# Performance work log

Measured on AMD Instinct MI355X. Metric: run time of the kernel, lower is better.

Reference implementation:

```python
import jax, jax.numpy as jnp
import numpy as np

N_QUBITS = 12
DEPTH = 4
OUT_DIM = 4096
BATCH = 2048
M_IN = 4096


def setup_inputs() -> dict:
    key = jax.random.key(0)
    k1, k2 = jax.random.split(key)
    x = jax.random.normal(k1, (BATCH, M_IN), dtype=jnp.float32)
    w = jax.random.uniform(k2, (DEPTH, N_QUBITS, 3), dtype=jnp.float32) * (2.0 * np.pi)
    return {"x": x, "w": w}


def _rot_matrix(phi, theta, omega):
    # PennyLane Rot(phi, theta, omega) = RZ(omega) @ RY(theta) @ RZ(phi)
    c = jnp.cos(theta / 2)
    s = jnp.sin(theta / 2)
    m = jnp.stack([
        jnp.stack([jnp.exp(-1j * (phi + omega) / 2) * c, -jnp.exp(1j * (phi - omega) / 2) * s]),
        jnp.stack([jnp.exp(-1j * (phi - omega) / 2) * s, jnp.exp(1j * (phi + omega) / 2) * c]),
    ])
    return m.astype(jnp.complex64)


def _apply_1q(s, U, q):
    # s: (B,) + (2,)*n ; wire q lives on axis q+1 (wire 0 = MSB, default.qubit order)
    s = jnp.moveaxis(s, q + 1, -1)
    s = jnp.einsum('...j,ij->...i', s, U)
    return jnp.moveaxis(s, -1, q + 1)


def _cnot(s, c, t):
    # control wire c < target wire t; flip target axis on the control=1 slice
    p0 = s[(slice(None),) * (c + 1) + (0,)]
    p1 = jnp.flip(s[(slice(None),) * (c + 1) + (1,)], axis=t)  # axis t after removing axis c+1
    return jnp.stack([p0, p1], axis=c + 1)


def _layer(s, wl):
    n = N_QUBITS
    for i in range(n):
        s = _apply_1q(s, _rot_matrix(wl[i, 0], wl[i, 1], wl[i, 2]), i)
    for i in range(n):
        for j in range(i + 1, n):
            s = _cnot(s, i, j)
    return s


def reference(x, w):
    B, m = x.shape
    n = N_QUBITS
    # amplitude embedding: per-sample L2 normalize with uniform fallback
    norm = jnp.linalg.norm(x, axis=1, keepdims=True)
    ok = norm > 1e-10
    amp = jnp.where(ok, x / jnp.where(ok, norm, 1.0), 1.0 / np.sqrt(m))
    s = amp.astype(jnp.complex64).reshape((B,) + (2,) * n)
    for layer in range(DEPTH):
        s = _layer(s, w[layer])
    sv = s.reshape(B, -1)
    probs = sv.real ** 2 + sv.imag ** 2
    pn = probs[:, :OUT_DIM]
    tot = jnp.sum(pn, axis=1, keepdims=True)
    okp = tot > 1e-10
    out = jnp.where(okp, pn / jnp.where(okp, tot, 1.0), 1.0 / OUT_DIM)
    return out.astype(x.dtype)
```

## Files before the change

kernel.cpp:

```cpp
#include <hip/hip_runtime.h>
#include <math.h>

#define NQ 12
#define DIM 4096
#define NLAYER 4
#define NT 512

typedef float v2 __attribute__((ext_vector_type(2)));

__device__ __forceinline__ v2 mkv2(float a, float b) { v2 r; r.x = a; r.y = b; return r; }
__device__ __forceinline__ v2 sp(float a) { v2 r; r.x = a; r.y = a; return r; }
__device__ __forceinline__ v2 pkfma(v2 a, float b, v2 c) {
  return __builtin_elementwise_fma(a, sp(b), c);
}

__device__ __forceinline__ int sfun(int z) {
  z ^= z >> 1; z ^= z >> 2; z ^= z >> 4; z ^= z >> 8; return z & (DIM - 1);
}
__device__ __forceinline__ int swz(int s) {
  int m = s ^ ((s >> 6) & 63);
  return m ^ ((m >> 3) & 7);
}

__device__ __forceinline__ v2 block_reduce_sum2(v2 v, v2* red) {
  const int tid = threadIdx.x;
#pragma unroll
  for (int off = 32; off > 0; off >>= 1) {
    v.x += __shfl_down(v.x, off, 64);
    v.y += __shfl_down(v.y, off, 64);
  }
  if ((tid & 63) == 0) red[tid >> 6] = v;
  __syncthreads();
  if (tid == 0) {
    v2 s = sp(0.f);
#pragma unroll
    for (int i = 0; i < NT / 64; ++i) s += red[i];
    red[0] = s;
  }
  __syncthreads();
  v2 r = red[0];
  __syncthreads();
  return r;
}

__device__ __forceinline__ void apply_pair(v2& r0, v2& i0, v2& r1, v2& i1,
    const float2 u00, const float2 u01, const float2 u10, const float2 u11) {
  v2 nr0 = pkfma(i1, -u01.y, pkfma(r1, u01.x, pkfma(i0, -u00.y, r0 * sp(u00.x))));
  v2 ni0 = pkfma(r1,  u01.y, pkfma(i1, u01.x, pkfma(r0,  u00.y, i0 * sp(u00.x))));
  v2 nr1 = pkfma(i1, -u11.y, pkfma(r1, u11.x, pkfma(i0, -u10.y, r0 * sp(u10.x))));
  v2 ni1 = pkfma(r1,  u11.y, pkfma(i1, u11.x, pkfma(r0,  u10.y, i0 * sp(u10.x))));
  r0 = nr0; i0 = ni0; r1 = nr1; i1 = ni1;
}

template <int RT>
__device__ __forceinline__ void gates3(v2 re[8], v2 im[8], const float2* GL) {
#pragma unroll
  for (int i = 0; i < 3; ++i) {
    const int q = 2 + 3 * RT - i;
    const float2 u00 = GL[q * 4 + 0], u01 = GL[q * 4 + 1];
    const float2 u10 = GL[q * 4 + 2], u11 = GL[q * 4 + 3];
#pragma unroll
    for (int pe = 0; pe < 4; ++pe) {
      const int e0 = ((pe >> i) << (i + 1)) | (pe & ((1 << i) - 1));
      const int e1 = e0 | (1 << i);
      apply_pair(re[e0], im[e0], re[e1], im[e1], u00, u01, u10, u11);
    }
  }
}

__global__ __launch_bounds__(NT, 4) void qsim_kernel(
    const float* __restrict__ x, const float* __restrict__ w,
    float* __restrict__ out) {
  extern __shared__ __align__(16) char smem[];
  float4* st   = (float4*)smem;
  float2* gmat = (float2*)(st + DIM);
  v2*     red  = (v2*)(gmat + NLAYER * NQ * 4);

  const int t = threadIdx.x;
  const int lane = t & 63, wave = t >> 6;
  const int a = t & 7, b = (t >> 3) & 7;
  const long r0 = 2L * blockIdx.x;

  if (t < NLAYER * NQ) {
    const float* wp = w + t * 3;
    float phi = wp[0], th = wp[1], om = wp[2];
    float sn, cc, sa, ca, sb, cb;
    sincosf(0.5f * th, &sn, &cc);
    sincosf(0.5f * (phi + om), &sa, &ca);
    sincosf(0.5f * (phi - om), &sb, &cb);
    float2* g = &gmat[t * 4];
    g[0] = make_float2(ca * cc, -sa * cc);
    g[1] = make_float2(-cb * sn, -sb * sn);
    g[2] = make_float2(cb * sn, -sb * sn);
    g[3] = make_float2(ca * cc, sa * cc);
  }

  const float4* xa = (const float4*)(x + r0 * DIM) + t * 2;
  const float4* xb = (const float4*)(x + (r0 + 1) * DIM) + t * 2;
  const float4 a0 = xa[0], a1 = xa[1], b0 = xb[0], b1 = xb[1];
  const float va[8] = {a0.x, a0.y, a0.z, a0.w, a1.x, a1.y, a1.z, a1.w};
  const float vb[8] = {b0.x, b0.y, b0.z, b0.w, b1.x, b1.y, b1.z, b1.w};
  v2 ss = sp(0.f);
#pragma unroll
  for (int e = 0; e < 8; ++e) { ss.x += va[e] * va[e]; ss.y += vb[e] * vb[e]; }
  const v2 nsq = block_reduce_sum2(ss, red);
  const float n0 = sqrtf(nsq.x), n1 = sqrtf(nsq.y);
  const bool ok0 = n0 > 1e-10f, ok1 = n1 > 1e-10f;
  const float i0f = ok0 ? 1.0f / n0 : 0.f, i1f = ok1 ? 1.0f / n1 : 0.f;
#pragma unroll
  for (int e = 0; e < 8; ++e)
    st[swz(t * 8 + e)] = make_float4(ok0 ? va[e] * i0f : 0.015625f,
                                     ok1 ? vb[e] * i1f : 0.015625f, 0.f, 0.f);

  int radr[8], gadr[8];
#pragma unroll
  for (int j = 0; j < 8; ++j) {
    radr[j] = swz(t | (j << 9));
    gadr[j] = swz(sfun(t | (j << 9)));
  }
  __syncthreads();

  v2 re[8], im[8];
#pragma unroll
  for (int L = 0; L < NLAYER; ++L) {
    const float2* GL = &gmat[L * NQ * 4];

#pragma unroll
    for (int j = 0; j < 8; ++j) {
      const float4 v = st[L == 0 ? radr[j] : gadr[j]];
      re[j] = mkv2(v.x, v.y); im[j] = mkv2(v.z, v.w);
    }
    gates3<0>(re, im, GL);
    __syncthreads();
#pragma unroll
    for (int j = 0; j < 8; ++j)
      st[swz(lane | (j << 6) | (wave << 9))] =
          make_float4(re[j].x, re[j].y, im[j].x, im[j].y);
    __syncthreads();

#pragma unroll
    for (int j = 0; j < 8; ++j) {
      const float4 v = st[radr[j]];
      re[j] = mkv2(v.x, v.y); im[j] = mkv2(v.z, v.w);
    }
    gates3<1>(re, im, GL);
    __syncthreads();
#pragma unroll
    for (int j = 0; j < 8; ++j)
      st[swz(a | (j << 3) | (wave << 6) | (b << 9))] =
          make_float4(re[j].x, re[j].y, im[j].x, im[j].y);
    __syncthreads();

#pragma unroll
    for (int j = 0; j < 8; ++j) {
      const float4 v = st[radr[j]];
      re[j] = mkv2(v.x, v.y); im[j] = mkv2(v.z, v.w);
    }
    gates3<2>(re, im, GL);
    __syncthreads();
#pragma unroll
    for (int j = 0; j < 8; ++j)
      st[swz(b | (j << 3) | (wave << 6) | (a << 9))] =
          make_float4(re[j].x, re[j].y, im[j].x, im[j].y);
    __syncthreads();

#pragma unroll
    for (int j = 0; j < 8; ++j) {
      const float4 v = st[radr[j]];
      re[j] = mkv2(v.x, v.y); im[j] = mkv2(v.z, v.w);
    }
    gates3<3>(re, im, GL);
    __syncthreads();
#pragma unroll
    for (int j = 0; j < 8; ++j)
      st[swz(j | (b << 3) | (a << 6) | (wave << 9))] =
          make_float4(re[j].x, re[j].y, im[j].x, im[j].y);
    __syncthreads();
  }

  float p0[8], p1[8];
  v2 ps = sp(0.f);
#pragma unroll
  for (int k = 0; k < 8; ++k) {
    const float4 v = st[gadr[k]];
    p0[k] = v.x * v.x + v.z * v.z;
    p1[k] = v.y * v.y + v.w * v.w;
    ps.x += p0[k]; ps.y += p1[k];
  }
  const v2 tot = block_reduce_sum2(ps, red);
  const bool k0 = tot.x > 1e-10f, k1 = tot.y > 1e-10f;
  const float t0 = k0 ? 1.0f / tot.x : 0.f, t1 = k1 ? 1.0f / tot.y : 0.f;
  float* o0 = out + r0 * DIM;
  float* o1 = out + (r0 + 1) * DIM;
#pragma unroll
  for (int k = 0; k < 8; ++k) {
    o0[t + k * NT] = k0 ? p0[k] * t0 : (1.0f / DIM);
    o1[t + k * NT] = k1 ? p1[k] * t1 : (1.0f / DIM);
  }
}

extern "C" void kernel_launch(void* const* d_in, const int* in_sizes, int n_in,
                              void* d_out, int out_size, void* d_ws, size_t ws_size,
                              hipStream_t stream) {
  const float* x = (const float*)d_in[0];
  const float* w = (const float*)d_in[1];
  float* out = (float*)d_out;
  const int B = in_sizes[0] / DIM;
  const size_t smem = DIM * sizeof(float4) + NLAYER * NQ * 4 * sizeof(float2)
                    + (NT / 64) * sizeof(v2);
  qsim_kernel<<<B / 2, NT, smem, stream>>>(x, w, out);
}
```

Baseline: 89.86 us.

## Write back to the same LDS slots each stage to drop barriers

Each gate stage now stores its amplitudes back to the same shared-memory addresses it just read, rather than to a permuted set. This removes the barrier between each stage's gates and its store in stages 1 to 3, and in stage 0 of the first layer. The permutations are moved into precomputed per-stage read-address arrays p0..p3. This cuts barriers per layer from about 8 to about 5, at the cost of more registers holding address arrays. Correctness depends on the new read-address chain reproducing the original qubit ordering across stages.

Result: faster. 87.55 us (-2.6%).

```diff
diff --git a/kernel.cpp b/kernel.cpp
--- a/kernel.cpp
+++ b/kernel.cpp
@@ -67,6 +67,18 @@
     }
   }
 }
+
+#define LOAD8(ADDR)                         \
+  _Pragma("unroll")                         \
+  for (int j = 0; j < 8; ++j) {             \
+    const float4 v = st[ADDR[j]];           \
+    re[j] = mkv2(v.x, v.y);                 \
+    im[j] = mkv2(v.z, v.w);                 \
+  }
+#define STORE8(ADDR)                        \
+  _Pragma("unroll")                         \
+  for (int j = 0; j < 8; ++j)               \
+    st[ADDR[j]] = make_float4(re[j].x, re[j].y, im[j].x, im[j].y);
 
 __global__ __launch_bounds__(NT, 4) void qsim_kernel(
     const float* __restrict__ x, const float* __restrict__ w,
@@ -112,11 +124,14 @@
     st[swz(t * 8 + e)] = make_float4(ok0 ? va[e] * i0f : 0.015625f,
                                      ok1 ? vb[e] * i1f : 0.015625f, 0.f, 0.f);
 
-  int radr[8], gadr[8];
+  int p0[8], p1[8], p2[8], p3[8], gd[8];
 #pragma unroll
   for (int j = 0; j < 8; ++j) {
-    radr[j] = swz(t | (j << 9));
-    gadr[j] = swz(sfun(t | (j << 9)));
+    p0[j] = swz(t | (j << 9));
+    p1[j] = swz(lane | (j << 6) | (wave << 9));
+    p2[j] = swz(a | (j << 3) | (b << 6) | (wave << 9));
+    p3[j] = swz(j | (a << 3) | (b << 6) | (wave << 9));
+    gd[j] = swz(sfun(t | (j << 9)));
   }
   __syncthreads();
 
@@ -125,67 +140,40 @@
   for (int L = 0; L < NLAYER; ++L) {
     const float2* GL = &gmat[L * NQ * 4];
 
-#pragma unroll
-    for (int j = 0; j < 8; ++j) {
-      const float4 v = st[L == 0 ? radr[j] : gadr[j]];
-      re[j] = mkv2(v.x, v.y); im[j] = mkv2(v.z, v.w);
+    if (L == 0) {
+      LOAD8(p0)
+    } else {
+      LOAD8(gd)
     }
     gates3<0>(re, im, GL);
-    __syncthreads();
-#pragma unroll
-    for (int j = 0; j < 8; ++j)
-      st[swz(lane | (j << 6) | (wave << 9))] =
-          make_float4(re[j].x, re[j].y, im[j].x, im[j].y);
-    __syncthreads();
-
-#pragma unroll
-    for (int j = 0; j < 8; ++j) {
-      const float4 v = st[radr[j]];
-      re[j] = mkv2(v.x, v.y); im[j] = mkv2(v.z, v.w);
-    }
+    if (L > 0) __syncthreads();
+    STORE8(p0)
+    __syncthreads();
+
+    LOAD8(p1)
     gates3<1>(re, im, GL);
-    __syncthreads();
-#pragma unroll
-    for (int j = 0; j < 8; ++j)
-      st[swz(a | (j << 3) | (wave << 6) | (b << 9))] =
-          make_float4(re[j].x, re[j].y, im[j].x, im[j].y);
-    __syncthreads();
-
-#pragma unroll
-    for (int j = 0; j < 8; ++j) {
-      const float4 v = st[radr[j]];
-      re[j] = mkv2(v.x, v.y); im[j] = mkv2(v.z, v.w);
-    }
+    STORE8(p1)
+    __syncthreads();
+
+    LOAD8(p2)
     gates3<2>(re, im, GL);
-    __syncthreads();
-#pragma unroll
-    for (int j = 0; j < 8; ++j)
-      st[swz(b | (j << 3) | (wave << 6) | (a << 9))] =
-          make_float4(re[j].x, re[j].y, im[j].x, im[j].y);
-    __syncthreads();
-
-#pragma unroll
-    for (int j = 0; j < 8; ++j) {
-      const float4 v = st[radr[j]];
-      re[j] = mkv2(v.x, v.y); im[j] = mkv2(v.z, v.w);
-    }
+    STORE8(p2)
+    __syncthreads();
+
+    LOAD8(p3)
     gates3<3>(re, im, GL);
-    __syncthreads();
-#pragma unroll
-    for (int j = 0; j < 8; ++j)
-      st[swz(j | (b << 3) | (a << 6) | (wave << 9))] =
-          make_float4(re[j].x, re[j].y, im[j].x, im[j].y);
-    __syncthreads();
-  }
-
-  float p0[8], p1[8];
+    STORE8(p3)
+    __syncthreads();
+  }
+
+  float q0[8], q1[8];
   v2 ps = sp(0.f);
 #pragma unroll
   for (int k = 0; k < 8; ++k) {
-    const float4 v = st[gadr[k]];
-    p0[k] = v.x * v.x + v.z * v.z;
-    p1[k] = v.y * v.y + v.w * v.w;
-    ps.x += p0[k]; ps.y += p1[k];
+    const float4 v = st[gd[k]];
+    q0[k] = v.x * v.x + v.z * v.z;
+    q1[k] = v.y * v.y + v.w * v.w;
+    ps.x += q0[k]; ps.y += q1[k];
   }
   const v2 tot = block_reduce_sum2(ps, red);
   const bool k0 = tot.x > 1e-10f, k1 = tot.y > 1e-10f;
@@ -194,8 +182,8 @@
   float* o1 = out + (r0 + 1) * DIM;
 #pragma unroll
   for (int k = 0; k < 8; ++k) {
-    o0[t + k * NT] = k0 ? p0[k] * t0 : (1.0f / DIM);
-    o1[t + k * NT] = k1 ? p1[k] * t1 : (1.0f / DIM);
+    o0[t + k * NT] = k0 ? q0[k] * t0 : (1.0f / DIM);
+    o1[t + k * NT] = k1 ? q1[k] * t1 : (1.0f / DIM);
   }
 }
 
```
